# Kernel optimization log

Measured on AMD Instinct MI355X. Metric: run time of the kernel, lower is better.

The kernel has to match this reference:

```python
import jax, jax.numpy as jnp
import numpy as np
from jax import lax

BN_EPS = 1e-5

def setup_inputs() -> dict:
    key = jax.random.key(0)
    k1, k2, k3, k4 = jax.random.split(key, 4)
    B, Cin, Cout, H, Wd = 32, 256, 256, 56, 56
    x = jax.random.normal(k1, (B, Cin, H, Wd), dtype=jnp.float32)
    gate = jax.random.uniform(k2, (B, Cin), dtype=jnp.float32)
    # expert convs: one 3x3 conv per input channel; stacked into a full OIHW kernel
    W = jax.random.normal(k3, (Cout, Cin, 3, 3), dtype=jnp.float32) * (1.0 / np.sqrt(Cin * 9))
    # per-expert bias: expert i contributes gate[:, i] * b_expert[i]
    b_expert = jax.random.normal(k4, (Cin, Cout), dtype=jnp.float32) * 0.01
    gamma = jnp.ones((Cout,), dtype=jnp.float32)
    beta = jnp.zeros((Cout,), dtype=jnp.float32)
    return {"x": x, "gate": gate, "W": W, "b_expert": b_expert, "gamma": gamma, "beta": beta}

def reference(x, gate, W, b_expert, gamma, beta):
    # MoELayer: sum_i gate[:, i] * conv_i(x[:, i:i+1]) == conv2d(x * gate, W_full)
    xg = x * gate[:, :, None, None]
    y = lax.conv_general_dilated(
        xg, W, window_strides=(1, 1), padding=((1, 1), (1, 1)),
        dimension_numbers=("NCHW", "OIHW", "NCHW"))
    bias = jnp.einsum("bi,io->bo", gate, b_expert)  # gate-weighted expert biases
    y = y + bias[:, :, None, None]
    # BatchNorm2d (training mode: batch statistics over N,H,W) + ReLU
    mean = jnp.mean(y, axis=(0, 2, 3))
    var = jnp.var(y, axis=(0, 2, 3))
    inv = lax.rsqrt(var + BN_EPS)
    y = (y - mean[None, :, None, None]) * (inv * gamma)[None, :, None, None] + beta[None, :, None, None]
    return jax.nn.relu(y)
```

## Files before the change

### kernel.cpp

```cpp
#include <hip/hip_runtime.h>
#include <cstdint>
#include <cstddef>

#define S_IMG   3136
#define PPOS    3364
#define PLANE_B (PPOS * 16)
#define XPAD_BYTES (32 * 8 * 4 * PLANE_B)
#define WT2_OFF    XPAD_BYTES
#define WT2_BYTES  (9 * 8 * 4 * 256 * 16)
#define STATS_OFF  (WT2_OFF + WT2_BYTES)

typedef __bf16 bf16x8 __attribute__((ext_vector_type(8)));
typedef short  s16x8  __attribute__((ext_vector_type(8)));
typedef float  f32x4  __attribute__((ext_vector_type(4)));

__device__ __forceinline__ unsigned short f2bf(float f) {
    unsigned u = __float_as_uint(f);
    u += 0x7fffu + ((u >> 16) & 1u);
    return (unsigned short)(u >> 16);
}

__device__ __forceinline__ void gll16(const void* g, void* l) {
    __builtin_amdgcn_global_load_lds(
        (const __attribute__((address_space(1))) void*)g,
        (__attribute__((address_space(3))) void*)l, 16, 0, 0);
}

__global__ __launch_bounds__(256) void zero_misc(char* __restrict__ xpad,
                                                 float* __restrict__ stats) {
    const int t = blockIdx.x * 256 + threadIdx.x;
    if (t < 1024 * 228) {
        const int plane = t / 228, pi = t % 228;
        int pos;
        if (pi < 58)       pos = pi;
        else if (pi < 116) pos = 3306 + (pi - 58);
        else { const int q = pi - 116; pos = ((q >> 1) + 1) * 58 + (q & 1) * 57; }
        *(uint4*)(xpad + (size_t)plane * PLANE_B + (size_t)pos * 16) =
            make_uint4(0u, 0u, 0u, 0u);
    } else if (t < 1024 * 228 + 1024) {
        stats[t - 1024 * 228] = 0.f;
    }
}

__global__ __launch_bounds__(256) void prep_x(const float* __restrict__ x,
                                              const float* __restrict__ gate,
                                              char* __restrict__ xpad) {
    __shared__ unsigned short xb[14336];
    const int tid = threadIdx.x;
    const int b = blockIdx.x / 56, h = blockIdx.x % 56;
    const float* xbase = x + (size_t)b * 256 * S_IMG + h * 56;
    const float* gb = gate + b * 256;
#pragma unroll
    for (int i = 0; i < 14; ++i) {
        const int e4 = i * 1024 + tid * 4;
        const int ci = e4 / 56, w = e4 % 56;
        const float4 v = *(const float4*)(xbase + (size_t)ci * S_IMG + w);
        const float g = gb[ci];
        ushort4 o;
        o.x = f2bf(v.x * g); o.y = f2bf(v.y * g);
        o.z = f2bf(v.z * g); o.w = f2bf(v.w * g);
        *(ushort4*)(xb + e4) = o;
    }
    __syncthreads();
    char* dst_b = xpad + (size_t)b * 32 * PLANE_B + ((size_t)((h + 1) * 58 + 1)) * 16;
#pragma unroll
    for (int i = 0; i < 7; ++i) {
        const int c = i * 256 + tid;
        const int pw = c % 56, cg = c / 56;
        const unsigned short* src = xb + cg * 8 * 56 + pw;
        uint4 o;
        o.x = (unsigned)src[0]   | ((unsigned)src[56]  << 16);
        o.y = (unsigned)src[112] | ((unsigned)src[168] << 16);
        o.z = (unsigned)src[224] | ((unsigned)src[280] << 16);
        o.w = (unsigned)src[336] | ((unsigned)src[392] << 16);
        *(uint4*)(dst_b + (size_t)cg * PLANE_B + (size_t)pw * 16) = o;
    }
}

__global__ __launch_bounds__(256) void prep_w(const float* __restrict__ W,
                                              char* __restrict__ wt2) {
    const int g = blockIdx.x * 256 + threadIdx.x;
    if (g >= 9 * 256 * 32) return;
    const int ci8 = g % 32;
    const int co  = (g / 32) % 256;
    const int tap = g / (32 * 256);
    const float* src = W + ((size_t)co * 256 + ci8 * 8) * 9 + tap;
    unsigned short v[8];
#pragma unroll
    for (int j = 0; j < 8; ++j) v[j] = f2bf(src[j * 9]);
    uint4 o;
    o.x = (unsigned)v[0] | ((unsigned)v[1] << 16);
    o.y = (unsigned)v[2] | ((unsigned)v[3] << 16);
    o.z = (unsigned)v[4] | ((unsigned)v[5] << 16);
    o.w = (unsigned)v[6] | ((unsigned)v[7] << 16);
    *(uint4*)(wt2 + ((size_t)(tap * 32 + ci8) * 256 + co) * 16) = o;
}

__global__ __launch_bounds__(256) void prep_bias(const float* __restrict__ gate,
                                                 const float* __restrict__ be,
                                                 float* __restrict__ bias) {
    const int b = blockIdx.x, co = threadIdx.x;
    const float* gb = gate + b * 256;
    float s = 0.f;
    for (int ci = 0; ci < 256; ++ci) s += gb[ci] * be[ci * 256 + co];
    bias[b * 256 + co] = s;
}

__global__ __launch_bounds__(256) void conv_mfma(
    const char* __restrict__ xpad, const char* __restrict__ wt2,
    const float* __restrict__ biasws, float* __restrict__ y,
    float* __restrict__ sums, float* __restrict__ sumsq) {
    __shared__ __align__(16) char smem[32768];
    const int tid = threadIdx.x;
    const int lane = tid & 63, wave = tid >> 6;
    const int wm = wave >> 1, wn = wave & 1;
    const int bi = blockIdx.x;
    const int co0 = (bi & 1) * 128;
    const int s0  = ((bi >> 1) % 25) * 128;
    const int b   = bi / 50;

    int sA = s0 + lane;       if (sA > S_IMG - 1) sA = S_IMG - 1;
    int sB = s0 + 64 + lane;  if (sB > S_IMG - 1) sB = S_IMG - 1;
    const int pA = sA + 59 + 2 * (sA / 56);
    const int pB = sB + 59 + 2 * (sB / 56);

    const int a_off = ((lane >> 4) * 2048) + (wm * 64 + (lane & 15)) * 16;
    const int b_off = 8192 + ((lane >> 4) * 2048) + (wn * 64 + (lane & 15)) * 16;

    f32x4 acc[4][4] = {};

    const char* xbase = xpad + (size_t)(b * 32 + wave) * PLANE_B;

    auto stage = [&](int k, int cur) {
        const int tap = k >> 3, cc = k & 7;
        const int off = (tap / 3) * 58 + (tap % 3) - 59;
        char* abase = smem + cur * 16384 + wave * 2048;
        char* bbase = abase + 8192;
        const char* asrc = wt2 + (size_t)((tap * 8 + cc) * 4 + wave) * 4096;
        gll16(asrc + (co0 + lane) * 16,      abase);
        gll16(asrc + (co0 + 64 + lane) * 16, abase + 1024);
        const char* bsrc = xbase + (size_t)cc * 4 * PLANE_B;
        gll16(bsrc + (pA + off) * 16, bbase);
        gll16(bsrc + (pB + off) * 16, bbase + 1024);
    };

    stage(0, 0);
    __syncthreads();

#pragma unroll 2
    for (int k = 0; k < 72; ++k) {
        const int cur = k & 1;
        if (k < 71) stage(k + 1, cur ^ 1);
        const char* base = smem + cur * 16384;
        s16x8 af[4], bfr[4];
#pragma unroll
        for (int m = 0; m < 4; ++m) af[m]  = *(const s16x8*)(base + a_off + m * 256);
#pragma unroll
        for (int n = 0; n < 4; ++n) bfr[n] = *(const s16x8*)(base + b_off + n * 256);
#pragma unroll
        for (int m = 0; m < 4; ++m)
#pragma unroll
            for (int n = 0; n < 4; ++n)
                acc[m][n] = __builtin_amdgcn_mfma_f32_16x16x32_bf16(
                    __builtin_bit_cast(bf16x8, af[m]),
                    __builtin_bit_cast(bf16x8, bfr[n]),
                    acc[m][n], 0, 0, 0);
        __syncthreads();
    }

    const int row_l = lane >> 4, col_l = lane & 15;
#pragma unroll
    for (int m = 0; m < 4; ++m) {
#pragma unroll
        for (int r = 0; r < 4; ++r) {
            const int co = co0 + wm * 64 + m * 16 + row_l * 4 + r;
            const float bv = biasws[b * 256 + co];
            float lsum = 0.f, lsq = 0.f;
#pragma unroll
            for (int n = 0; n < 4; ++n) {
                const int s = s0 + wn * 64 + n * 16 + col_l;
                if (s < S_IMG) {
                    const float v = acc[m][n][r] + bv;
                    y[(size_t)(b * 256 + co) * S_IMG + s] = v;
                    lsum += v; lsq += v * v;
                }
            }
#pragma unroll
            for (int d = 1; d < 16; d <<= 1) {
                lsum += __shfl_xor(lsum, d, 64);
                lsq  += __shfl_xor(lsq,  d, 64);
            }
            if (col_l == 0) {
                atomicAdd(&sums[co],  lsum);
                atomicAdd(&sumsq[co], lsq);
            }
        }
    }
}

__global__ void bn_finalize(const float* __restrict__ sums,
                            const float* __restrict__ sumsq,
                            const float* __restrict__ gamma,
                            const float* __restrict__ beta,
                            float* __restrict__ scale, float* __restrict__ shift) {
    const int co = threadIdx.x;
    const float inv_n = 1.f / (float)(32 * S_IMG);
    const float mean = sums[co] * inv_n;
    const float var  = sumsq[co] * inv_n - mean * mean;
    const float inv  = rsqrtf(var + 1e-5f);
    const float sc   = gamma[co] * inv;
    scale[co] = sc;
    shift[co] = beta[co] - mean * sc;
}

__global__ __launch_bounds__(256) void bn_apply(float* __restrict__ y,
                                                const float* __restrict__ scale,
                                                const float* __restrict__ shift) {
    const size_t i = (size_t)blockIdx.x * 256 + threadIdx.x;
    const int co = (int)((i / 784) & 255);
    float4 v = ((const float4*)y)[i];
    const float sc = scale[co], sh = shift[co];
    v.x = fmaxf(v.x * sc + sh, 0.f);
    v.y = fmaxf(v.y * sc + sh, 0.f);
    v.z = fmaxf(v.z * sc + sh, 0.f);
    v.w = fmaxf(v.w * sc + sh, 0.f);
    ((float4*)y)[i] = v;
}

extern "C" void kernel_launch(void* const* d_in, const int* in_sizes, int n_in,
                              void* d_out, int out_size, void* d_ws, size_t ws_size,
                              hipStream_t stream) {
    const float* x     = (const float*)d_in[0];
    const float* gate  = (const float*)d_in[1];
    const float* W     = (const float*)d_in[2];
    const float* be    = (const float*)d_in[3];
    const float* gamma = (const float*)d_in[4];
    const float* beta  = (const float*)d_in[5];
    float* y  = (float*)d_out;
    char*  ws = (char*)d_ws;

    char* xpad = ws;
    char* wt2  = ws + WT2_OFF;
    float* stats = (float*)(ws + STATS_OFF);
    float* sums  = stats;
    float* sumsq = stats + 256;
    float* scale = stats + 512;
    float* shift = stats + 768;
    float* bias  = stats + 1024;

    hipLaunchKernelGGL(zero_misc,  dim3(917),   dim3(256), 0, stream, xpad, stats);
    hipLaunchKernelGGL(prep_x,     dim3(32*56), dim3(256), 0, stream, x, gate, xpad);
    hipLaunchKernelGGL(prep_w,     dim3(288),   dim3(256), 0, stream, W, wt2);
    hipLaunchKernelGGL(prep_bias,  dim3(32),    dim3(256), 0, stream, gate, be, bias);
    hipLaunchKernelGGL(conv_mfma,  dim3(1600),  dim3(256), 0, stream,
                       xpad, wt2, bias, y, sums, sumsq);
    hipLaunchKernelGGL(bn_finalize,dim3(1),     dim3(256), 0, stream,
                       sums, sumsq, gamma, beta, scale, shift);
    hipLaunchKernelGGL(bn_apply,   dim3(25088), dim3(256), 0, stream, y, scale, shift);
}
```

Measured before the change: 556.5 us.

## Triple-buffer conv pipeline, XCD-aware block mapping, and merge prep/finalize kernels

```diff
diff --git a/kernel.cpp b/kernel.cpp
--- a/kernel.cpp
+++ b/kernel.cpp
@@ -26,19 +26,48 @@
         (__attribute__((address_space(3))) void*)l, 16, 0, 0);
 }
 
-__global__ __launch_bounds__(256) void zero_misc(char* __restrict__ xpad,
-                                                 float* __restrict__ stats) {
-    const int t = blockIdx.x * 256 + threadIdx.x;
-    if (t < 1024 * 228) {
-        const int plane = t / 228, pi = t % 228;
-        int pos;
-        if (pi < 58)       pos = pi;
-        else if (pi < 116) pos = 3306 + (pi - 58);
-        else { const int q = pi - 116; pos = ((q >> 1) + 1) * 58 + (q & 1) * 57; }
-        *(uint4*)(xpad + (size_t)plane * PLANE_B + (size_t)pos * 16) =
-            make_uint4(0u, 0u, 0u, 0u);
-    } else if (t < 1024 * 228 + 1024) {
-        stats[t - 1024 * 228] = 0.f;
+__global__ __launch_bounds__(256) void prep_small(const float* __restrict__ W,
+                                                  const float* __restrict__ gate,
+                                                  const float* __restrict__ be,
+                                                  char* __restrict__ xpad,
+                                                  char* __restrict__ wt2,
+                                                  float* __restrict__ stats) {
+    const int blk = blockIdx.x;
+    if (blk < 917) {
+        const int t = blk * 256 + threadIdx.x;
+        if (t < 1024 * 228) {
+            const int plane = t / 228, pi = t % 228;
+            int pos;
+            if (pi < 58)       pos = pi;
+            else if (pi < 116) pos = 3306 + (pi - 58);
+            else { const int q = pi - 116; pos = ((q >> 1) + 1) * 58 + (q & 1) * 57; }
+            *(uint4*)(xpad + (size_t)plane * PLANE_B + (size_t)pos * 16) =
+                make_uint4(0u, 0u, 0u, 0u);
+        } else if (t < 1024 * 228 + 512) {
+            stats[t - 1024 * 228] = 0.f;
+        }
+    } else if (blk < 1205) {
+        const int g = (blk - 917) * 256 + threadIdx.x;
+        if (g >= 9 * 256 * 32) return;
+        const int ci8 = g % 32;
+        const int co  = (g / 32) % 256;
+        const int tap = g / (32 * 256);
+        const float* src = W + ((size_t)co * 256 + ci8 * 8) * 9 + tap;
+        unsigned short v[8];
+#pragma unroll
+        for (int j = 0; j < 8; ++j) v[j] = f2bf(src[j * 9]);
+        uint4 o;
+        o.x = (unsigned)v[0] | ((unsigned)v[1] << 16);
+        o.y = (unsigned)v[2] | ((unsigned)v[3] << 16);
+        o.z = (unsigned)v[4] | ((unsigned)v[5] << 16);
+        o.w = (unsigned)v[6] | ((unsigned)v[7] << 16);
+        *(uint4*)(wt2 + ((size_t)(tap * 32 + ci8) * 256 + co) * 16) = o;
+    } else {
+        const int b = blk - 1205, co = threadIdx.x;
+        const float* gb = gate + b * 256;
+        float s = 0.f;
+        for (int ci = 0; ci < 256; ++ci) s += gb[ci] * be[ci * 256 + co];
+        stats[512 + b * 256 + co] = s;
     }
 }
 
@@ -77,47 +106,21 @@
     }
 }
 
-__global__ __launch_bounds__(256) void prep_w(const float* __restrict__ W,
-                                              char* __restrict__ wt2) {
-    const int g = blockIdx.x * 256 + threadIdx.x;
-    if (g >= 9 * 256 * 32) return;
-    const int ci8 = g % 32;
-    const int co  = (g / 32) % 256;
-    const int tap = g / (32 * 256);
-    const float* src = W + ((size_t)co * 256 + ci8 * 8) * 9 + tap;
-    unsigned short v[8];
-#pragma unroll
-    for (int j = 0; j < 8; ++j) v[j] = f2bf(src[j * 9]);
-    uint4 o;
-    o.x = (unsigned)v[0] | ((unsigned)v[1] << 16);
-    o.y = (unsigned)v[2] | ((unsigned)v[3] << 16);
-    o.z = (unsigned)v[4] | ((unsigned)v[5] << 16);
-    o.w = (unsigned)v[6] | ((unsigned)v[7] << 16);
-    *(uint4*)(wt2 + ((size_t)(tap * 32 + ci8) * 256 + co) * 16) = o;
-}
-
-__global__ __launch_bounds__(256) void prep_bias(const float* __restrict__ gate,
-                                                 const float* __restrict__ be,
-                                                 float* __restrict__ bias) {
-    const int b = blockIdx.x, co = threadIdx.x;
-    const float* gb = gate + b * 256;
-    float s = 0.f;
-    for (int ci = 0; ci < 256; ++ci) s += gb[ci] * be[ci * 256 + co];
-    bias[b * 256 + co] = s;
-}
-
 __global__ __launch_bounds__(256) void conv_mfma(
     const char* __restrict__ xpad, const char* __restrict__ wt2,
     const float* __restrict__ biasws, float* __restrict__ y,
     float* __restrict__ sums, float* __restrict__ sumsq) {
-    __shared__ __align__(16) char smem[32768];
+    __shared__ __align__(16) char smem[49152];
     const int tid = threadIdx.x;
     const int lane = tid & 63, wave = tid >> 6;
     const int wm = wave >> 1, wn = wave & 1;
-    const int bi = blockIdx.x;
-    const int co0 = (bi & 1) * 128;
-    const int s0  = ((bi >> 1) % 25) * 128;
-    const int b   = bi / 50;
+
+    const int L = blockIdx.x;
+    const int xcd = L & 7, j = L >> 3;
+    const int p   = xcd * 100 + (j >> 1);
+    const int co0 = (j & 1) * 128;
+    const int b   = p / 25;
+    const int s0  = (p % 25) * 128;
 
     int sA = s0 + lane;       if (sA > S_IMG - 1) sA = S_IMG - 1;
     int sB = s0 + 64 + lane;  if (sB > S_IMG - 1) sB = S_IMG - 1;
@@ -131,10 +134,10 @@
 
     const char* xbase = xpad + (size_t)(b * 32 + wave) * PLANE_B;
 
-    auto stage = [&](int k, int cur) {
-        const int tap = k >> 3, cc = k & 7;
+    auto stage = [&](int k, int bufidx) {
+        const int cc = k / 9, tap = k - cc * 9;
         const int off = (tap / 3) * 58 + (tap % 3) - 59;
-        char* abase = smem + cur * 16384 + wave * 2048;
+        char* abase = smem + bufidx * 16384 + wave * 2048;
         char* bbase = abase + 8192;
         const char* asrc = wt2 + (size_t)((tap * 8 + cc) * 4 + wave) * 4096;
         gll16(asrc + (co0 + lane) * 16,      abase);
@@ -145,18 +148,24 @@
     };
 
     stage(0, 0);
-    __syncthreads();
-
-#pragma unroll 2
+    stage(1, 1);
+
+#pragma unroll 3
     for (int k = 0; k < 72; ++k) {
-        const int cur = k & 1;
-        if (k < 71) stage(k + 1, cur ^ 1);
-        const char* base = smem + cur * 16384;
+        if (k < 70) asm volatile("s_waitcnt vmcnt(4)" ::: "memory");
+        else        asm volatile("s_waitcnt vmcnt(0)" ::: "memory");
+        __builtin_amdgcn_sched_barrier(0);
+        __builtin_amdgcn_s_barrier();
+        __builtin_amdgcn_sched_barrier(0);
+        if (k + 2 < 72) stage(k + 2, (k + 2) % 3);
+
+        const char* base = smem + (k % 3) * 16384;
         s16x8 af[4], bfr[4];
 #pragma unroll
         for (int m = 0; m < 4; ++m) af[m]  = *(const s16x8*)(base + a_off + m * 256);
 #pragma unroll
         for (int n = 0; n < 4; ++n) bfr[n] = *(const s16x8*)(base + b_off + n * 256);
+        __builtin_amdgcn_s_setprio(1);
 #pragma unroll
         for (int m = 0; m < 4; ++m)
 #pragma unroll
@@ -165,7 +174,7 @@
                     __builtin_bit_cast(bf16x8, af[m]),
                     __builtin_bit_cast(bf16x8, bfr[n]),
                     acc[m][n], 0, 0, 0);
-        __syncthreads();
+        __builtin_amdgcn_s_setprio(0);
     }
 
     const int row_l = lane >> 4, col_l = lane & 15;
@@ -198,28 +207,19 @@
     }
 }
 
-__global__ void bn_finalize(const float* __restrict__ sums,
-                            const float* __restrict__ sumsq,
-                            const float* __restrict__ gamma,
-                            const float* __restrict__ beta,
-                            float* __restrict__ scale, float* __restrict__ shift) {
-    const int co = threadIdx.x;
+__global__ __launch_bounds__(256) void bn_apply(float* __restrict__ y,
+                                                const float* __restrict__ sums,
+                                                const float* __restrict__ sumsq,
+                                                const float* __restrict__ gamma,
+                                                const float* __restrict__ beta) {
+    const size_t i = (size_t)blockIdx.x * 256 + threadIdx.x;
+    const int co = (int)((i / 784) & 255);
     const float inv_n = 1.f / (float)(32 * S_IMG);
     const float mean = sums[co] * inv_n;
     const float var  = sumsq[co] * inv_n - mean * mean;
-    const float inv  = rsqrtf(var + 1e-5f);
-    const float sc   = gamma[co] * inv;
-    scale[co] = sc;
-    shift[co] = beta[co] - mean * sc;
-}
-
-__global__ __launch_bounds__(256) void bn_apply(float* __restrict__ y,
-                                                const float* __restrict__ scale,
-                                                const float* __restrict__ shift) {
-    const size_t i = (size_t)blockIdx.x * 256 + threadIdx.x;
-    const int co = (int)((i / 784) & 255);
+    const float sc   = gamma[co] * rsqrtf(var + 1e-5f);
+    const float sh   = beta[co] - mean * sc;
     float4 v = ((const float4*)y)[i];
-    const float sc = scale[co], sh = shift[co];
     v.x = fmaxf(v.x * sc + sh, 0.f);
     v.y = fmaxf(v.y * sc + sh, 0.f);
     v.z = fmaxf(v.z * sc + sh, 0.f);
@@ -244,17 +244,13 @@
     float* stats = (float*)(ws + STATS_OFF);
     float* sums  = stats;
     float* sumsq = stats + 256;
-    float* scale = stats + 512;
-    float* shift = stats + 768;
-    float* bias  = stats + 1024;
-
-    hipLaunchKernelGGL(zero_misc,  dim3(917),   dim3(256), 0, stream, xpad, stats);
+    float* bias  = stats + 512;
+
+    hipLaunchKernelGGL(prep_small, dim3(1237),  dim3(256), 0, stream,
+                       W, gate, be, xpad, wt2, stats);
     hipLaunchKernelGGL(prep_x,     dim3(32*56), dim3(256), 0, stream, x, gate, xpad);
-    hipLaunchKernelGGL(prep_w,     dim3(288),   dim3(256), 0, stream, W, wt2);
-    hipLaunchKernelGGL(prep_bias,  dim3(32),    dim3(256), 0, stream, gate, be, bias);
     hipLaunchKernelGGL(conv_mfma,  dim3(1600),  dim3(256), 0, stream,
                        xpad, wt2, bias, y, sums, sumsq);
-    hipLaunchKernelGGL(bn_finalize,dim3(1),     dim3(256), 0, stream,
-                       sums, sumsq, gamma, beta, scale, shift);
-    hipLaunchKernelGGL(bn_apply,   dim3(25088), dim3(256), 0, stream, y, scale, shift);
-}
+    hipLaunchKernelGGL(bn_apply,   dim3(25088), dim3(256), 0, stream,
+                       y, sums, sumsq, gamma, beta);
+}
```

Measured after the change: 470.9 us. 15.4% less time.
